# Kernel tuning notes

Measured on AMD Instinct MI355X. Metric: run time of the kernel, lower is better.

Reference implementation:

```python
import jax, jax.numpy as jnp
import numpy as np

IN_CH = 256
NUM_ANCHORS = 9
NUM_CLASSES = 80
FEAT_SHAPES = [(4, IN_CH, 100, 100), (4, IN_CH, 50, 50), (4, IN_CH, 25, 25), (4, IN_CH, 13, 13), (4, IN_CH, 7, 7)]


def conv3x3(x, w, b):
    # x: [N,C,H,W], w: [O,I,3,3] (OIHW), stride 1, SAME padding
    y = jax.lax.conv_general_dilated(x, w, window_strides=(1, 1), padding='SAME',
                                     dimension_numbers=('NCHW', 'OIHW', 'NCHW'))
    return y + b[None, :, None, None]


def head_branch(x, conv_w, conv_b, out_w, out_b, K):
    for i in range(4):
        x = jax.nn.relu(conv3x3(x, conv_w[i], conv_b[i]))
    y = conv3x3(x, out_w, out_b)
    N, AK, H, W = y.shape
    A = AK // K
    return y.reshape(N, A, K, H, W).transpose(0, 3, 4, 1, 2).reshape(N, H * W * A, K)


def setup_inputs() -> dict:
    key = jax.random.key(0)
    ks = jax.random.split(key, 16)
    inp = {}
    for i, shp in enumerate(FEAT_SHAPES):
        inp[f'feat{i}'] = jax.random.normal(ks[i], shp, dtype=jnp.float32)
    std = 0.01  # torch init: normal(std=0.01), zero bias
    inp['cls_conv_w'] = jax.random.normal(ks[5], (4, IN_CH, IN_CH, 3, 3), dtype=jnp.float32) * std
    inp['cls_conv_b'] = jnp.zeros((4, IN_CH), dtype=jnp.float32)
    inp['cls_out_w'] = jax.random.normal(ks[6], (NUM_ANCHORS * NUM_CLASSES, IN_CH, 3, 3), dtype=jnp.float32) * std
    prior = 0.01
    inp['cls_out_b'] = jnp.full((NUM_ANCHORS * NUM_CLASSES,), -np.log((1.0 - prior) / prior), dtype=jnp.float32)
    inp['reg_conv_w'] = jax.random.normal(ks[7], (4, IN_CH, IN_CH, 3, 3), dtype=jnp.float32) * std
    inp['reg_conv_b'] = jnp.zeros((4, IN_CH), dtype=jnp.float32)
    inp['reg_out_w'] = jax.random.normal(ks[8], (NUM_ANCHORS * 4, IN_CH, 3, 3), dtype=jnp.float32) * std
    inp['reg_out_b'] = jnp.zeros((NUM_ANCHORS * 4,), dtype=jnp.float32)
    return inp


def reference(feat0, feat1, feat2, feat3, feat4,
              cls_conv_w, cls_conv_b, cls_out_w, cls_out_b,
              reg_conv_w, reg_conv_b, reg_out_w, reg_out_b):
    feats = [feat0, feat1, feat2, feat3, feat4]
    cls_logits = jnp.concatenate(
        [head_branch(f, cls_conv_w, cls_conv_b, cls_out_w, cls_out_b, NUM_CLASSES) for f in feats], axis=1)
    bbox_regression = jnp.concatenate(
        [head_branch(f, reg_conv_w, reg_conv_b, reg_out_w, reg_out_b, 4) for f in feats], axis=1)
    return cls_logits, bbox_regression
```

## Files before the change

### kernel.cpp

```cpp
#include <hip/hip_runtime.h>


typedef __bf16 v8bf __attribute__((ext_vector_type(8)));
typedef float f32x4 __attribute__((ext_vector_type(4)));

__device__ __forceinline__ v8bf zero8() {
  v8bf v;
#pragma unroll
  for (int j = 0; j < 8; ++j) v[j] = (__bf16)0.0f;
  return v;
}

__device__ __forceinline__ void glds16(const void* g, void* l) {
  __builtin_amdgcn_global_load_lds((const __attribute__((address_space(1))) unsigned int*)g,
                                   (__attribute__((address_space(3))) unsigned int*)l, 16, 0, 0);
}

__global__ __launch_bounds__(256)
void prep_in(const float* __restrict__ f0, const float* __restrict__ f1,
             const float* __restrict__ f2, const float* __restrict__ f3,
             const float* __restrict__ f4, __bf16* __restrict__ dst)
{
  int oct = blockIdx.x * 256 + threadIdx.x;
  if (oct >= 1707904) return;
  int el = oct << 3;
  int c0 = el & 255;
  int pix = el >> 8;
  const float* s; int HW, hw, n;
  if (pix < 40000)      { s = f0; HW = 10000; int p = pix;         n = p / 10000; hw = p - n * 10000; }
  else if (pix < 50000) { s = f1; HW = 2500;  int p = pix - 40000; n = p / 2500;  hw = p - n * 2500;  }
  else if (pix < 52500) { s = f2; HW = 625;   int p = pix - 50000; n = p / 625;   hw = p - n * 625;   }
  else if (pix < 53176) { s = f3; HW = 169;   int p = pix - 52500; n = p / 169;   hw = p - n * 169;   }
  else                  { s = f4; HW = 49;    int p = pix - 53176; n = p / 49;    hw = p - n * 49;    }
  const float* sp = s + (n * 256 + c0) * HW + hw;
  v8bf v;
#pragma unroll
  for (int j = 0; j < 8; ++j) v[j] = (__bf16)sp[j * HW];
  *(v8bf*)(dst + el) = v;
}

__global__ __launch_bounds__(256)
void prep_w(const float* __restrict__ src, __bf16* __restrict__ dst, int NTp, int CO)
{
  int t = blockIdx.x * 256 + threadIdx.x;
  int total = NTp * 8 * 9 * 128 * 4;
  if (t >= total) return;
  int p = t & 3;
  int x = t >> 2;
  int co = x & 127; x >>= 7;
  int tap = x % 9; x /= 9;
  int cc = x & 7; int nt = x >> 3;
  int l = p ^ ((co >> 1) & 3);
  int cog = nt * 128 + co;
  v8bf v = zero8();
  if (cog < CO) {
    const float* sp = src + ((size_t)cog * 256 + cc * 32 + l * 8) * 9 + tap;
#pragma unroll
    for (int j = 0; j < 8; ++j) v[j] = (__bf16)sp[j * 9];
  }
  *(v8bf*)(dst + ((size_t)(((nt * 8 + cc) * 9 + tap) * 128 + co) * 32 + p * 8)) = v;
}

template<int MODE>
__global__ __launch_bounds__(256, 3)
void conv_k(const __bf16* __restrict__ src, __bf16* __restrict__ dstA,
            float* __restrict__ dstF, const __bf16* __restrict__ wbuf,
            const float* __restrict__ bias, const __bf16* __restrict__ zpg,
            int NT, int CO)
{
  __shared__ __align__(16) char lds[49152];
  char* ldsA = lds;
  char* ldsB = lds + 32768;

  int bid = blockIdx.x;
  int nt = bid % NT, mt = bid / NT;
  int n = mt / 107, r = mt - n * 107;
  int W, H, HW, pbase, ob, t;
  if (MODE == 1) {
    if (r < 79)       { W=100;H=100;HW=10000;pbase=0;     ob=0;       t=r; }
    else if (r < 99)  { W=50; H=50; HW=2500; pbase=40000; ob=7200000; t=r-79; }
    else if (r < 104) { W=25; H=25; HW=625;  pbase=50000; ob=9000000; t=r-99; }
    else if (r < 106) { W=13; H=13; HW=169;  pbase=52500; ob=9450000; t=r-104; }
    else              { W=7;  H=7;  HW=49;   pbase=53176; ob=9571680; t=r-106; }
  } else {
    if (r < 79)       { W=100;H=100;HW=10000;pbase=0;     ob=0;      t=r; }
    else if (r < 99)  { W=50; H=50; HW=2500; pbase=40000; ob=360000; t=r-79; }
    else if (r < 104) { W=25; H=25; HW=625;  pbase=50000; ob=450000; t=r-99; }
    else if (r < 106) { W=13; H=13; HW=169;  pbase=52500; ob=472500; t=r-104; }
    else              { W=7;  H=7;  HW=49;   pbase=53176; ob=478584; t=r-106; }
  }
  int p0 = t << 7;
  int npx = HW - p0; if (npx > 128) npx = 128;
  int pend = p0 + npx - 1;
  int Wp = W + 2;
  int rowlo = p0 / W - 1;

  int tid = threadIdx.x, lane = tid & 63, wv = tid >> 6;
  int wm = wv >> 1, wn = wv & 1, la = lane & 15, kg = lane >> 4;
  int i0 = wv * 8;

  const char* addrA[8];
#pragma unroll
  for (int j = 0; j < 8; ++j) {
    int i = i0 + j;
    int pos = i * 16 + (lane >> 2);
    int h = pos / Wp;
    int wc = pos - h * Wp - 1;
    int ar = rowlo + h;
    int pl = (lane & 3) ^ ((pos >> 1) & 3);
    bool ok = (ar >= 0) & (ar < H) & (wc >= 0) & (wc < W);
    addrA[j] = ok ? (const char*)(src + (((size_t)(pbase + n * HW + ar * W + wc)) << 8) + pl * 8)
                  : (const char*)zpg + (lane & 3) * 16;
  }

  int pos0[4];
  int fvalid[4];
#pragma unroll
  for (int f = 0; f < 4; ++f) {
    int fg = wm * 4 + f;
    fvalid[f] = (fg * 16 < npx);
    int p = p0 + fg * 16 + la; if (p > pend) p = pend;
    int h = p / W, w = p - h * W;
    pos0[f] = (h - rowlo) * Wp + (w + 1);
  }

  const char* bsrc = (const char*)wbuf + (size_t)nt * 589824 + wv * 2048 + lane * 16;

  f32x4 acc[4][4];
#pragma unroll
  for (int f = 0; f < 4; ++f)
#pragma unroll
    for (int j = 0; j < 4; ++j)
#pragma unroll
      for (int k = 0; k < 4; ++k) acc[f][j][k] = 0.0f;

#define ISSUE_A() do { _Pragma("unroll") \
    for (int j = 0; j < 8; ++j) { glds16(addrA[j], ldsA + (i0 + j) * 1024); addrA[j] += 64; } } while (0)
#define ISSUE_B(q, buf) do { const char* s_ = bsrc + (q) * 8192; \
    char* d_ = ldsB + (buf) * 8192 + wv * 2048; \
    glds16(s_, d_); glds16(s_ + 1024, d_ + 1024); } while (0)

  ISSUE_A();
  ISSUE_B(0, 0);
  int pb = 0;

  for (int cc = 0; cc < 8; ++cc) {
#pragma unroll
    for (int tap = 0; tap < 9; ++tap) {
      __syncthreads();
      int q = cc * 9 + tap;
      if (q < 71) ISSUE_B(q + 1, pb ^ 1);
      const int dh = tap / 3 - 1, dw = tap % 3 - 1;
      int dt = dh * Wp + dw;
      v8bf bfr[4];
#pragma unroll
      for (int nj = 0; nj < 4; ++nj) {
        int co = wn * 64 + nj * 16 + la;
        int bb = ((co << 6) + (kg << 4)) ^ (((co >> 1) & 3) << 4);
        bfr[nj] = *(const v8bf*)(ldsB + pb * 8192 + bb);
      }
#pragma unroll
      for (int f = 0; f < 4; ++f) {
        if (fvalid[f]) {
          int pos = pos0[f] + dt;
          int ab = ((pos << 6) + (kg << 4)) ^ (((pos >> 1) & 3) << 4);
          v8bf af = *(const v8bf*)(ldsA + ab);
#pragma unroll
          for (int nj = 0; nj < 4; ++nj)
            acc[f][nj] = __builtin_amdgcn_mfma_f32_16x16x32_bf16(af, bfr[nj], acc[f][nj], 0, 0, 0);
        }
      }
      pb ^= 1;
      if (tap == 8 && cc < 7) { __syncthreads(); ISSUE_A(); }
    }
  }

#pragma unroll
  for (int f = 0; f < 4; ++f) {
    int fg = wm * 4 + f;
    if (fg * 16 < npx) {
#pragma unroll
      for (int nj = 0; nj < 4; ++nj) {
        int cob = nt * 128 + wn * 64 + nj * 16 + la;
        float bs = (cob < CO) ? bias[cob] : 0.0f;
#pragma unroll
        for (int rr = 0; rr < 4; ++rr) {
          int pl = fg * 16 + kg * 4 + rr;
          if (pl < npx) {
            float vv = acc[f][nj][rr] + bs;
            int pix = p0 + pl;
            if (MODE == 0) {
              vv = fmaxf(vv, 0.0f);
              dstA[(((size_t)(pbase + n * HW + pix)) << 8) + cob] = (__bf16)vv;
            } else if (MODE == 1) {
              if (cob < 720)
                dstF[(size_t)n * 9606960 + ob + (size_t)pix * 720 + cob] = vv;
            } else {
              if (cob < 36)
                dstF[38427840 + (size_t)n * 480348 + ob + (size_t)pix * 36 + cob] = vv;
            }
          }
        }
      }
    }
  }
#undef ISSUE_A
#undef ISSUE_B
}

extern "C" void kernel_launch(void* const* d_in, const int* in_sizes, int n_in,
                              void* d_out, int out_size, void* d_ws, size_t ws_size,
                              hipStream_t stream) {
  (void)in_sizes; (void)n_in; (void)out_size; (void)ws_size;
  const float* feat0 = (const float*)d_in[0];
  const float* feat1 = (const float*)d_in[1];
  const float* feat2 = (const float*)d_in[2];
  const float* feat3 = (const float*)d_in[3];
  const float* feat4 = (const float*)d_in[4];
  const float* cls_w  = (const float*)d_in[5];
  const float* cls_b  = (const float*)d_in[6];
  const float* cls_ow = (const float*)d_in[7];
  const float* cls_ob = (const float*)d_in[8];
  const float* reg_w  = (const float*)d_in[9];
  const float* reg_b  = (const float*)d_in[10];
  const float* reg_ow = (const float*)d_in[11];
  const float* reg_ob = (const float*)d_in[12];
  float* out = (float*)d_out;

  const int ACT = 13663232;
  const int WT  = 589824;
  __bf16* base    = (__bf16*)d_ws;
  __bf16* in_nhwc = base;
  __bf16* actA    = base + ACT;
  __bf16* actB    = base + 2 * ACT;
  __bf16* wb      = base + 3 * ACT;
  __bf16* wb_cls[4], *wb_reg[4];
  for (int li = 0; li < 4; ++li) { wb_cls[li] = wb + li * WT; wb_reg[li] = wb + (4 + li) * WT; }
  __bf16* wb_co = wb + 8 * WT;
  __bf16* wb_ro = wb_co + 1769472;
  __bf16* zpg   = wb_ro + 294912;

  hipMemsetAsync(zpg, 0, 8192, stream);
  prep_in<<<6672, 256, 0, stream>>>(feat0, feat1, feat2, feat3, feat4, in_nhwc);
  for (int li = 0; li < 4; ++li) {
    prep_w<<<288, 256, 0, stream>>>(cls_w + li * WT, wb_cls[li], 2, 256);
    prep_w<<<288, 256, 0, stream>>>(reg_w + li * WT, wb_reg[li], 2, 256);
  }
  prep_w<<<864, 256, 0, stream>>>(cls_ow, wb_co, 6, 720);
  prep_w<<<144, 256, 0, stream>>>(reg_ow, wb_ro, 1, 36);

  const int GT = 428 * 2;
  conv_k<0><<<GT, 256, 0, stream>>>(in_nhwc, actA, nullptr, wb_cls[0], cls_b + 0,   zpg, 2, 256);
  conv_k<0><<<GT, 256, 0, stream>>>(actA,    actB, nullptr, wb_cls[1], cls_b + 256, zpg, 2, 256);
  conv_k<0><<<GT, 256, 0, stream>>>(actB,    actA, nullptr, wb_cls[2], cls_b + 512, zpg, 2, 256);
  conv_k<0><<<GT, 256, 0, stream>>>(actA,    actB, nullptr, wb_cls[3], cls_b + 768, zpg, 2, 256);
  conv_k<1><<<428 * 6, 256, 0, stream>>>(actB, nullptr, out, wb_co, cls_ob, zpg, 6, 720);
  conv_k<0><<<GT, 256, 0, stream>>>(in_nhwc, actA, nullptr, wb_reg[0], reg_b + 0,   zpg, 2, 256);
  conv_k<0><<<GT, 256, 0, stream>>>(actA,    actB, nullptr, wb_reg[1], reg_b + 256, zpg, 2, 256);
  conv_k<0><<<GT, 256, 0, stream>>>(actB,    actA, nullptr, wb_reg[2], reg_b + 512, zpg, 2, 256);
  conv_k<0><<<GT, 256, 0, stream>>>(actA,    actB, nullptr, wb_reg[3], reg_b + 768, zpg, 2, 256);
  conv_k<2><<<428, 256, 0, stream>>>(actB, nullptr, out, wb_ro, reg_ob, zpg, 1, 36);
}
```

Before: 1.160 ms.

## Fuse cls/reg tower launches, load weights directly to registers, swizzle block order

```diff
diff --git a/kernel.cpp b/kernel.cpp
--- a/kernel.cpp
+++ b/kernel.cpp
@@ -14,6 +14,17 @@
 __device__ __forceinline__ void glds16(const void* g, void* l) {
   __builtin_amdgcn_global_load_lds((const __attribute__((address_space(1))) unsigned int*)g,
                                    (__attribute__((address_space(3))) unsigned int*)l, 16, 0, 0);
+}
+
+struct Geo { int W, H, HW, pbase, obC, obR, t; };
+__device__ __forceinline__ Geo decode(int r) {
+  Geo g;
+  if (r < 79)       { g.W=100;g.H=100;g.HW=10000;g.pbase=0;     g.obC=0;       g.obR=0;      g.t=r; }
+  else if (r < 99)  { g.W=50; g.H=50; g.HW=2500; g.pbase=40000; g.obC=7200000; g.obR=360000; g.t=r-79; }
+  else if (r < 104) { g.W=25; g.H=25; g.HW=625;  g.pbase=50000; g.obC=9000000; g.obR=450000; g.t=r-99; }
+  else if (r < 106) { g.W=13; g.H=13; g.HW=169;  g.pbase=52500; g.obC=9450000; g.obR=472500; g.t=r-104; }
+  else              { g.W=7;  g.H=7;  g.HW=49;   g.pbase=53176; g.obC=9571680; g.obR=478584; g.t=r-106; }
+  return g;
 }
 
 __global__ __launch_bounds__(256)
@@ -40,125 +51,90 @@
 }
 
 __global__ __launch_bounds__(256)
-void prep_w(const float* __restrict__ src, __bf16* __restrict__ dst, int NTp, int CO)
+void prep_w_all(const float* __restrict__ cls_w, const float* __restrict__ reg_w,
+                const float* __restrict__ cls_ow, const float* __restrict__ reg_ow,
+                __bf16* __restrict__ wb)
 {
   int t = blockIdx.x * 256 + threadIdx.x;
-  int total = NTp * 8 * 9 * 128 * 4;
-  if (t >= total) return;
-  int p = t & 3;
-  int x = t >> 2;
-  int co = x & 127; x >>= 7;
-  int tap = x % 9; x /= 9;
-  int cc = x & 7; int nt = x >> 3;
-  int l = p ^ ((co >> 1) & 3);
+  const float* src; __bf16* dst; int CO, within;
+  if (t < 589824) {
+    int tensor = t / 73728; within = t % 73728;
+    src = tensor < 4 ? cls_w + tensor * 589824 : reg_w + (tensor - 4) * 589824;
+    dst = wb + (size_t)tensor * 589824; CO = 256;
+  } else if (t < 811008) {
+    within = t - 589824; src = cls_ow; dst = wb + 8 * 589824; CO = 720;
+  } else {
+    within = t - 811008; src = reg_ow; dst = wb + 8 * 589824 + 1769472; CO = 36;
+  }
+  int p = within & 3; int xx = within >> 2;
+  int co = xx & 127; xx >>= 7;
+  int tap = xx % 9; xx /= 9;
+  int cc = xx & 7; int nt = xx >> 3;
   int cog = nt * 128 + co;
   v8bf v = zero8();
   if (cog < CO) {
-    const float* sp = src + ((size_t)cog * 256 + cc * 32 + l * 8) * 9 + tap;
+    const float* sp = src + ((size_t)cog * 256 + cc * 32 + p * 8) * 9 + tap;
 #pragma unroll
     for (int j = 0; j < 8; ++j) v[j] = (__bf16)sp[j * 9];
   }
   *(v8bf*)(dst + ((size_t)(((nt * 8 + cc) * 9 + tap) * 128 + co) * 32 + p * 8)) = v;
 }
 
-template<int MODE>
-__global__ __launch_bounds__(256, 3)
-void conv_k(const __bf16* __restrict__ src, __bf16* __restrict__ dstA,
-            float* __restrict__ dstF, const __bf16* __restrict__ wbuf,
-            const float* __restrict__ bias, const __bf16* __restrict__ zpg,
-            int NT, int CO)
-{
-  __shared__ __align__(16) char lds[49152];
-  char* ldsA = lds;
-  char* ldsB = lds + 32768;
-
-  int bid = blockIdx.x;
-  int nt = bid % NT, mt = bid / NT;
-  int n = mt / 107, r = mt - n * 107;
-  int W, H, HW, pbase, ob, t;
-  if (MODE == 1) {
-    if (r < 79)       { W=100;H=100;HW=10000;pbase=0;     ob=0;       t=r; }
-    else if (r < 99)  { W=50; H=50; HW=2500; pbase=40000; ob=7200000; t=r-79; }
-    else if (r < 104) { W=25; H=25; HW=625;  pbase=50000; ob=9000000; t=r-99; }
-    else if (r < 106) { W=13; H=13; HW=169;  pbase=52500; ob=9450000; t=r-104; }
-    else              { W=7;  H=7;  HW=49;   pbase=53176; ob=9571680; t=r-106; }
-  } else {
-    if (r < 79)       { W=100;H=100;HW=10000;pbase=0;     ob=0;      t=r; }
-    else if (r < 99)  { W=50; H=50; HW=2500; pbase=40000; ob=360000; t=r-79; }
-    else if (r < 104) { W=25; H=25; HW=625;  pbase=50000; ob=450000; t=r-99; }
-    else if (r < 106) { W=13; H=13; HW=169;  pbase=52500; ob=472500; t=r-104; }
-    else              { W=7;  H=7;  HW=49;   pbase=53176; ob=478584; t=r-106; }
-  }
-  int p0 = t << 7;
-  int npx = HW - p0; if (npx > 128) npx = 128;
-  int pend = p0 + npx - 1;
-  int Wp = W + 2;
-  int rowlo = p0 / W - 1;
-
-  int tid = threadIdx.x, lane = tid & 63, wv = tid >> 6;
-  int wm = wv >> 1, wn = wv & 1, la = lane & 15, kg = lane >> 4;
-  int i0 = wv * 8;
-
-  const char* addrA[8];
+__device__ __forceinline__ void conv_core(const char* __restrict__ wsbase,
+    unsigned so, unsigned zpoff, const __bf16* __restrict__ wnt,
+    int W, int H, int p0, int npx, f32x4 (&acc)[4][4])
+{
+  __shared__ __align__(16) char ldsA[32768];
+  const int Wp = W + 2;
+  const int pend = p0 + npx - 1;
+  const int rowlo = p0 / W - 1;
+  const int tid = threadIdx.x, lane = tid & 63, wv = tid >> 6;
+  const int wn = wv & 1, wm = wv >> 1, la = lane & 15, kg = lane >> 4;
+  const int i0 = wv * 8;
+
+  unsigned offA[8];
 #pragma unroll
   for (int j = 0; j < 8; ++j) {
-    int i = i0 + j;
-    int pos = i * 16 + (lane >> 2);
+    int pos = (i0 + j) * 16 + (lane >> 2);
     int h = pos / Wp;
     int wc = pos - h * Wp - 1;
     int ar = rowlo + h;
     int pl = (lane & 3) ^ ((pos >> 1) & 3);
     bool ok = (ar >= 0) & (ar < H) & (wc >= 0) & (wc < W);
-    addrA[j] = ok ? (const char*)(src + (((size_t)(pbase + n * HW + ar * W + wc)) << 8) + pl * 8)
-                  : (const char*)zpg + (lane & 3) * 16;
-  }
-
-  int pos0[4];
-  int fvalid[4];
+    offA[j] = ok ? (so + (unsigned)(ar * W + wc) * 512u + (unsigned)pl * 16u)
+                 : (zpoff + (unsigned)(lane & 3) * 16u);
+  }
+
+  int pos0[4], fvalid[4];
 #pragma unroll
   for (int f = 0; f < 4; ++f) {
     int fg = wm * 4 + f;
     fvalid[f] = (fg * 16 < npx);
     int p = p0 + fg * 16 + la; if (p > pend) p = pend;
-    int h = p / W, w = p - h * W;
-    pos0[f] = (h - rowlo) * Wp + (w + 1);
-  }
-
-  const char* bsrc = (const char*)wbuf + (size_t)nt * 589824 + wv * 2048 + lane * 16;
-
-  f32x4 acc[4][4];
-#pragma unroll
-  for (int f = 0; f < 4; ++f)
-#pragma unroll
-    for (int j = 0; j < 4; ++j)
-#pragma unroll
-      for (int k = 0; k < 4; ++k) acc[f][j][k] = 0.0f;
-
-#define ISSUE_A() do { _Pragma("unroll") \
-    for (int j = 0; j < 8; ++j) { glds16(addrA[j], ldsA + (i0 + j) * 1024); addrA[j] += 64; } } while (0)
-#define ISSUE_B(q, buf) do { const char* s_ = bsrc + (q) * 8192; \
-    char* d_ = ldsB + (buf) * 8192 + wv * 2048; \
-    glds16(s_, d_); glds16(s_ + 1024, d_ + 1024); } while (0)
-
-  ISSUE_A();
-  ISSUE_B(0, 0);
-  int pb = 0;
+    int h = p / W;
+    pos0[f] = (h - rowlo) * Wp + (p - h * W + 1);
+  }
+
+  const __bf16* bgl = wnt + ((wn * 64 + la) << 5) + (kg << 3);
+  v8bf bcur[4], bnxt[4];
+#pragma unroll
+  for (int nj = 0; nj < 4; ++nj) bcur[nj] = *(const v8bf*)(bgl + nj * 512);
 
   for (int cc = 0; cc < 8; ++cc) {
+    __syncthreads();
+#pragma unroll
+    for (int j = 0; j < 8; ++j) { glds16(wsbase + offA[j], (char*)ldsA + (i0 + j) * 1024); offA[j] += 64u; }
+    __syncthreads();
 #pragma unroll
     for (int tap = 0; tap < 9; ++tap) {
-      __syncthreads();
       int q = cc * 9 + tap;
-      if (q < 71) ISSUE_B(q + 1, pb ^ 1);
+      if (q < 71) {
+        const __bf16* nb = bgl + (q + 1) * 4096;
+#pragma unroll
+        for (int nj = 0; nj < 4; ++nj) bnxt[nj] = *(const v8bf*)(nb + nj * 512);
+      }
       const int dh = tap / 3 - 1, dw = tap % 3 - 1;
-      int dt = dh * Wp + dw;
-      v8bf bfr[4];
-#pragma unroll
-      for (int nj = 0; nj < 4; ++nj) {
-        int co = wn * 64 + nj * 16 + la;
-        int bb = ((co << 6) + (kg << 4)) ^ (((co >> 1) & 3) << 4);
-        bfr[nj] = *(const v8bf*)(ldsB + pb * 8192 + bb);
-      }
+      const int dt = dh * Wp + dw;
 #pragma unroll
       for (int f = 0; f < 4; ++f) {
         if (fvalid[f]) {
@@ -167,14 +143,52 @@
           v8bf af = *(const v8bf*)(ldsA + ab);
 #pragma unroll
           for (int nj = 0; nj < 4; ++nj)
-            acc[f][nj] = __builtin_amdgcn_mfma_f32_16x16x32_bf16(af, bfr[nj], acc[f][nj], 0, 0, 0);
+            acc[f][nj] = __builtin_amdgcn_mfma_f32_16x16x32_bf16(af, bcur[nj], acc[f][nj], 0, 0, 0);
         }
       }
-      pb ^= 1;
-      if (tap == 8 && cc < 7) { __syncthreads(); ISSUE_A(); }
+#pragma unroll
+      for (int nj = 0; nj < 4; ++nj) bcur[nj] = bnxt[nj];
     }
   }
-
+}
+
+__global__ __launch_bounds__(256, 4)
+void conv_tower(const char* __restrict__ wsbase,
+                unsigned so0, __bf16* __restrict__ dst0, const __bf16* __restrict__ w0, const float* __restrict__ b0,
+                unsigned so1, __bf16* __restrict__ dst1, const __bf16* __restrict__ w1, const float* __restrict__ b1,
+                unsigned zpoff, int nb)
+{
+  int bid = blockIdx.x;
+  int br = (nb == 2 && bid >= 864) ? 1 : 0;
+  bid -= br * 864;
+  unsigned soff = br ? so1 : so0;
+  __bf16* dst = br ? dst1 : dst0;
+  const __bf16* wt = br ? w1 : w0;
+  const float* bias = br ? b1 : b0;
+
+  int x = bid & 7, slot = bid >> 3;
+  int nt = slot & 1, mtl = slot >> 1;
+  int mt = x + (mtl << 3);
+  if (mt >= 428) return;
+  int n = mt / 107, r = mt - n * 107;
+  Geo g = decode(r);
+  int p0 = g.t << 7;
+  int npx = g.HW - p0; if (npx > 128) npx = 128;
+  unsigned so = soff + (unsigned)(g.pbase + n * g.HW) * 512u;
+
+  f32x4 acc[4][4];
+#pragma unroll
+  for (int f = 0; f < 4; ++f)
+#pragma unroll
+    for (int j = 0; j < 4; ++j)
+#pragma unroll
+      for (int k = 0; k < 4; ++k) acc[f][j][k] = 0.0f;
+
+  conv_core(wsbase, so, zpoff, wt + nt * 294912, g.W, g.H, p0, npx, acc);
+
+  int lane = threadIdx.x & 63, wv = threadIdx.x >> 6;
+  int wm = wv >> 1, wn = wv & 1, la = lane & 15, kg = lane >> 4;
+  size_t pixbase = (size_t)(g.pbase + n * g.HW + p0);
 #pragma unroll
   for (int f = 0; f < 4; ++f) {
     int fg = wm * 4 + f;
@@ -182,36 +196,83 @@
 #pragma unroll
       for (int nj = 0; nj < 4; ++nj) {
         int cob = nt * 128 + wn * 64 + nj * 16 + la;
-        float bs = (cob < CO) ? bias[cob] : 0.0f;
+        float bs = bias[cob];
+#pragma unroll
+        for (int rr = 0; rr < 4; ++rr) {
+          int pl = fg * 16 + kg * 4 + rr;
+          if (pl < npx)
+            dst[((pixbase + pl) << 8) + cob] = (__bf16)fmaxf(acc[f][nj][rr] + bs, 0.0f);
+        }
+      }
+    }
+  }
+}
+
+__global__ __launch_bounds__(256, 4)
+void conv_out(const char* __restrict__ wsbase, unsigned soC, unsigned soR,
+              float* __restrict__ out, const __bf16* __restrict__ wco, const float* __restrict__ bco,
+              const __bf16* __restrict__ wro, const float* __restrict__ bro,
+              unsigned zpoff, int do_cls)
+{
+  int bid = blockIdx.x;
+  int isreg = 0;
+  if (do_cls) { if (bid >= 2592) { isreg = 1; bid -= 2592; } }
+  else isreg = 1;
+
+  int x = bid & 7, slot = bid >> 3;
+  int nt, mtl;
+  if (!isreg) { nt = slot % 6; mtl = slot / 6; } else { nt = 0; mtl = slot; }
+  int mt = x + mtl * 8;
+  if (mt >= 428) return;
+  int n = mt / 107, r = mt - n * 107;
+  Geo g = decode(r);
+  int p0 = g.t << 7;
+  int npx = g.HW - p0; if (npx > 128) npx = 128;
+  unsigned so = (isreg ? soR : soC) + (unsigned)(g.pbase + n * g.HW) * 512u;
+  const __bf16* wnt = isreg ? wro : (wco + nt * 294912);
+
+  f32x4 acc[4][4];
+#pragma unroll
+  for (int f = 0; f < 4; ++f)
+#pragma unroll
+    for (int j = 0; j < 4; ++j)
+#pragma unroll
+      for (int k = 0; k < 4; ++k) acc[f][j][k] = 0.0f;
+
+  conv_core(wsbase, so, zpoff, wnt, g.W, g.H, p0, npx, acc);
+
+  int lane = threadIdx.x & 63, wv = threadIdx.x >> 6;
+  int wm = wv >> 1, wn = wv & 1, la = lane & 15, kg = lane >> 4;
+#pragma unroll
+  for (int f = 0; f < 4; ++f) {
+    int fg = wm * 4 + f;
+    if (fg * 16 < npx) {
+#pragma unroll
+      for (int nj = 0; nj < 4; ++nj) {
+        int cob = nt * 128 + wn * 64 + nj * 16 + la;
 #pragma unroll
         for (int rr = 0; rr < 4; ++rr) {
           int pl = fg * 16 + kg * 4 + rr;
           if (pl < npx) {
-            float vv = acc[f][nj][rr] + bs;
             int pix = p0 + pl;
-            if (MODE == 0) {
-              vv = fmaxf(vv, 0.0f);
-              dstA[(((size_t)(pbase + n * HW + pix)) << 8) + cob] = (__bf16)vv;
-            } else if (MODE == 1) {
+            if (!isreg) {
               if (cob < 720)
-                dstF[(size_t)n * 9606960 + ob + (size_t)pix * 720 + cob] = vv;
+                out[(size_t)n * 9606960 + g.obC + (size_t)pix * 720 + cob] = acc[f][nj][rr] + bco[cob];
             } else {
               if (cob < 36)
-                dstF[38427840 + (size_t)n * 480348 + ob + (size_t)pix * 36 + cob] = vv;
+                out[38427840 + (size_t)n * 480348 + g.obR + (size_t)pix * 36 + cob] = acc[f][nj][rr] + bro[cob];
             }
           }
         }
       }
     }
   }
-#undef ISSUE_A
-#undef ISSUE_B
 }
 
 extern "C" void kernel_launch(void* const* d_in, const int* in_sizes, int n_in,
                               void* d_out, int out_size, void* d_ws, size_t ws_size,
                               hipStream_t stream) {
-  (void)in_sizes; (void)n_in; (void)out_size; (void)ws_size;
+  (void)in_sizes; (void)n_in; (void)out_size;
   const float* feat0 = (const float*)d_in[0];
   const float* feat1 = (const float*)d_in[1];
   const float* feat2 = (const float*)d_in[2];
@@ -227,37 +288,52 @@
   const float* reg_ob = (const float*)d_in[12];
   float* out = (float*)d_out;
 
-  const int ACT = 13663232;
-  const int WT  = 589824;
-  __bf16* base    = (__bf16*)d_ws;
-  __bf16* in_nhwc = base;
-  __bf16* actA    = base + ACT;
-  __bf16* actB    = base + 2 * ACT;
-  __bf16* wb      = base + 3 * ACT;
-  __bf16* wb_cls[4], *wb_reg[4];
-  for (int li = 0; li < 4; ++li) { wb_cls[li] = wb + li * WT; wb_reg[li] = wb + (4 + li) * WT; }
-  __bf16* wb_co = wb + 8 * WT;
-  __bf16* wb_ro = wb_co + 1769472;
-  __bf16* zpg   = wb_ro + 294912;
-
-  hipMemsetAsync(zpg, 0, 8192, stream);
-  prep_in<<<6672, 256, 0, stream>>>(feat0, feat1, feat2, feat3, feat4, in_nhwc);
-  for (int li = 0; li < 4; ++li) {
-    prep_w<<<288, 256, 0, stream>>>(cls_w + li * WT, wb_cls[li], 2, 256);
-    prep_w<<<288, 256, 0, stream>>>(reg_w + li * WT, wb_reg[li], 2, 256);
-  }
-  prep_w<<<864, 256, 0, stream>>>(cls_ow, wb_co, 6, 720);
-  prep_w<<<144, 256, 0, stream>>>(reg_ow, wb_ro, 1, 36);
-
-  const int GT = 428 * 2;
-  conv_k<0><<<GT, 256, 0, stream>>>(in_nhwc, actA, nullptr, wb_cls[0], cls_b + 0,   zpg, 2, 256);
-  conv_k<0><<<GT, 256, 0, stream>>>(actA,    actB, nullptr, wb_cls[1], cls_b + 256, zpg, 2, 256);
-  conv_k<0><<<GT, 256, 0, stream>>>(actB,    actA, nullptr, wb_cls[2], cls_b + 512, zpg, 2, 256);
-  conv_k<0><<<GT, 256, 0, stream>>>(actA,    actB, nullptr, wb_cls[3], cls_b + 768, zpg, 2, 256);
-  conv_k<1><<<428 * 6, 256, 0, stream>>>(actB, nullptr, out, wb_co, cls_ob, zpg, 6, 720);
-  conv_k<0><<<GT, 256, 0, stream>>>(in_nhwc, actA, nullptr, wb_reg[0], reg_b + 0,   zpg, 2, 256);
-  conv_k<0><<<GT, 256, 0, stream>>>(actA,    actB, nullptr, wb_reg[1], reg_b + 256, zpg, 2, 256);
-  conv_k<0><<<GT, 256, 0, stream>>>(actB,    actA, nullptr, wb_reg[2], reg_b + 512, zpg, 2, 256);
-  conv_k<0><<<GT, 256, 0, stream>>>(actA,    actB, nullptr, wb_reg[3], reg_b + 768, zpg, 2, 256);
-  conv_k<2><<<428, 256, 0, stream>>>(actB, nullptr, out, wb_ro, reg_ob, zpg, 1, 36);
-}
+  const size_t ACT = 13663232;
+  const size_t WSEG = 6782976;
+  const char* wsbase = (const char*)d_ws;
+  __bf16* base = (__bf16*)d_ws;
+
+  bool fused = ws_size >= (5 * ACT + WSEG + 4096) * 2;
+  int nact = fused ? 5 : 3;
+  __bf16* A = base + ACT;
+  __bf16* B = base + 2 * ACT;
+  __bf16* C = fused ? base + 3 * ACT : A;
+  __bf16* D = fused ? base + 4 * ACT : B;
+  __bf16* wb = base + nact * ACT;
+  __bf16* zp = wb + WSEG;
+
+  __bf16* w_cls[4], *w_reg[4];
+  for (int li = 0; li < 4; ++li) { w_cls[li] = wb + (size_t)li * 589824; w_reg[li] = wb + (size_t)(4 + li) * 589824; }
+  __bf16* wco = wb + 8 * 589824;
+  __bf16* wro = wco + 1769472;
+
+  unsigned off_in = 0;
+  unsigned off_A = (unsigned)(ACT * 2);
+  unsigned off_B = (unsigned)(ACT * 4);
+  unsigned off_C = fused ? (unsigned)(ACT * 6) : off_A;
+  unsigned off_D = fused ? (unsigned)(ACT * 8) : off_B;
+  unsigned off_zp = (unsigned)((nact * ACT + WSEG) * 2);
+
+  hipMemsetAsync(zp, 0, 8192, stream);
+  prep_in<<<6672, 256, 0, stream>>>(feat0, feat1, feat2, feat3, feat4, base);
+  prep_w_all<<<3312, 256, 0, stream>>>(cls_w, reg_w, cls_ow, reg_ow, wb);
+
+  if (fused) {
+    conv_tower<<<1728, 256, 0, stream>>>(wsbase, off_in, A, w_cls[0], cls_b + 0,   off_in, C, w_reg[0], reg_b + 0,   off_zp, 2);
+    conv_tower<<<1728, 256, 0, stream>>>(wsbase, off_A,  B, w_cls[1], cls_b + 256, off_C,  D, w_reg[1], reg_b + 256, off_zp, 2);
+    conv_tower<<<1728, 256, 0, stream>>>(wsbase, off_B,  A, w_cls[2], cls_b + 512, off_D,  C, w_reg[2], reg_b + 512, off_zp, 2);
+    conv_tower<<<1728, 256, 0, stream>>>(wsbase, off_A,  B, w_cls[3], cls_b + 768, off_C,  D, w_reg[3], reg_b + 768, off_zp, 2);
+    conv_out<<<3024, 256, 0, stream>>>(wsbase, off_B, off_D, out, wco, cls_ob, wro, reg_ob, off_zp, 1);
+  } else {
+    conv_tower<<<864, 256, 0, stream>>>(wsbase, off_in, A, w_cls[0], cls_b + 0,   0, A, w_cls[0], cls_b, off_zp, 1);
+    conv_tower<<<864, 256, 0, stream>>>(wsbase, off_A,  B, w_cls[1], cls_b + 256, 0, A, w_cls[0], cls_b, off_zp, 1);
+    conv_tower<<<864, 256, 0, stream>>>(wsbase, off_B,  A, w_cls[2], cls_b + 512, 0, A, w_cls[0], cls_b, off_zp, 1);
+    conv_tower<<<864, 256, 0, stream>>>(wsbase, off_A,  B, w_cls[3], cls_b + 768, 0, A, w_cls[0], cls_b, off_zp, 1);
+    conv_out<<<2592, 256, 0, stream>>>(wsbase, off_B, off_B, out, wco, cls_ob, wro, reg_ob, off_zp, 1);
+    conv_tower<<<864, 256, 0, stream>>>(wsbase, off_in, A, w_reg[0], reg_b + 0,   0, A, w_reg[0], reg_b, off_zp, 1);
+    conv_tower<<<864, 256, 0, stream>>>(wsbase, off_A,  B, w_reg[1], reg_b + 256, 0, A, w_reg[0], reg_b, off_zp, 1);
+    conv_tower<<<864, 256, 0, stream>>>(wsbase, off_B,  A, w_reg[2], reg_b + 512, 0, A, w_reg[0], reg_b, off_zp, 1);
+    conv_tower<<<864, 256, 0, stream>>>(wsbase, off_A,  B, w_reg[3], reg_b + 768, 0, A, w_reg[0], reg_b, off_zp, 1);
+    conv_out<<<432, 256, 0, stream>>>(wsbase, off_B, off_B, out, wco, cls_ob, wro, reg_ob, off_zp, 0);
+  }
+}
```

After: 1.849 ms. 1.59x slower.
